# Optimization experiments

Measured on AMD Instinct MI355X. Metric: run time of the kernel, lower is better.

The kernel has to match this reference:

```python
import jax, jax.numpy as jnp
import numpy as np

SIGMA = 1.0          # influence distance of kernel points
KERNEL_RADIUS = 1.0  # radius within which kernel points live


def setup_inputs() -> dict:
    key = jax.random.key(0)
    k0, k1, k2, k3, k4 = jax.random.split(key, 5)
    B, M, K_NB, D_IN, D_OUT, K_PTS = 4, 16384, 32, 64, 64, 15
    X = jax.random.normal(k0, (B, M, 3), dtype=jnp.float32)          # point coords
    F = jax.random.normal(k1, (B, M, D_IN), dtype=jnp.float32)        # point features
    N = jax.random.randint(k2, (B, M, K_NB), 0, M)                    # neighbor indices
    Q = jax.random.uniform(k3, (K_PTS, 3), minval=-KERNEL_RADIUS,
                           maxval=KERNEL_RADIUS, dtype=jnp.float32)   # kernel points
    W = jax.random.normal(k4, (K_PTS, D_IN, D_OUT), dtype=jnp.float32) * 0.05
    return {"X": X, "F": F, "N": N, "Q": Q, "W": W}


def reference(X, F, N, Q, W):
    # Gather neighbor coordinates and features: [B, M, k, 3] / [B, M, k, d_in]
    gather = jax.vmap(lambda a, idx: a[idx])
    Xn = gather(X, N)
    Fn = gather(F, N)
    # Relative neighbor positions w.r.t. each center point
    r = Xn - X[:, :, None, :]                                  # [B, M, k, 3]
    # Distance of each relative position to each kernel point
    d = jnp.linalg.norm(r[:, :, :, None, :] - Q, axis=-1)      # [B, M, k, Kp]
    # Linear correlation influence (KPConv)
    h = jnp.maximum(0.0, 1.0 - d / SIGMA)                      # [B, M, k, Kp]
    # Distance-weighted neighbor aggregation per kernel point
    Fk = jnp.einsum('bmkp,bmkd->bmpd', h, Fn)                  # [B, M, Kp, d_in]
    # Per-kernel-point linear maps, summed over kernel points
    return jnp.einsum('bmpd,pde->bme', Fk, W)                  # [B, M, d_out]
```

## Files before the change

### kernel.cpp

```cpp
#include <hip/hip_runtime.h>
#include <hip/hip_bf16.h>


#define BATCH 4
#define MPTS  16384
#define KNB   32
#define DIN   64
#define DOUT  64
#define KP    15
#define K2P   1024
#define KSTEPS (K2P/32)
#define ROWB  (K2P*2)
#define PTS   (BATCH*MPTS)
#define PPB   16
#define NBLK  (PTS/PPB)
#define WBELEMS (K2P*DOUT)

typedef __bf16 bf16x8 __attribute__((ext_vector_type(8)));
typedef float  f32x4  __attribute__((ext_vector_type(4)));
typedef unsigned short u16x8 __attribute__((ext_vector_type(8)));

static __device__ __forceinline__ unsigned short f2b(float x) {
    __bf16 h = (__bf16)x;
    return __builtin_bit_cast(unsigned short, h);
}

__global__ void prep_wb(const float* __restrict__ W, unsigned short* __restrict__ wb) {
    int idx = blockIdx.x * 256 + threadIdx.x;
    if (idx >= WBELEMS) return;
    int i    = idx & 7;
    int lane = (idx >> 3) & 63;
    int ks   = (idx >> 9) & 31;
    int et   = idx >> 14;
    int kap  = ks * 32 + ((lane >> 4) << 3) + i;
    int n = kap >> 6;
    int g = (kap >> 4) & 3;
    int t = (kap >> 2) & 3;
    int r = kap & 3;
    int p = g * 4 + r;
    int d = n * 4 + t;
    int e = et * 16 + (lane & 15);
    float v = (p < KP) ? W[(p * DIN + d) * DOUT + e] : 0.f;
    wb[idx] = f2b(v);
}

__global__ void f2bf_kernel(const float* __restrict__ src, unsigned short* __restrict__ dst, int n8) {
    int i = blockIdx.x * 256 + threadIdx.x;
    if (i >= n8) return;
    const float4* s = reinterpret_cast<const float4*>(src) + (size_t)i * 2;
    float4 a = s[0], b = s[1];
    u16x8 o;
    o[0] = f2b(a.x); o[1] = f2b(a.y); o[2] = f2b(a.z); o[3] = f2b(a.w);
    o[4] = f2b(b.x); o[5] = f2b(b.y); o[6] = f2b(b.z); o[7] = f2b(b.w);
    *(reinterpret_cast<u16x8*>(dst) + i) = o;
}

__global__ __launch_bounds__(256, 5)
void kpconv_main(const float* __restrict__ X, const unsigned short* __restrict__ FB,
                 const int* __restrict__ NB, const float* __restrict__ Q,
                 const unsigned short* __restrict__ WB, float* __restrict__ OUT) {
    __shared__ unsigned short fk[16 * K2P];

    char* const fkb = reinterpret_cast<char*>(fk);

    const int tid  = threadIdx.x;
    const int wv   = tid >> 6;
    const int lane = tid & 63;
    const int g16  = lane >> 4;
    const int r16  = lane & 15;

    float qx = 1.0e3f, qy = 0.f, qz = 0.f;
    if (r16 < KP) { qx = Q[r16 * 3 + 0]; qy = Q[r16 * 3 + 1]; qz = Q[r16 * 3 + 2]; }
    const float qq   = qx * qx + qy * qy + qz * qz;
    const float nq2x = -2.f * qx, nq2y = -2.f * qy, nq2z = -2.f * qz;

    const int bid     = blockIdx.x;
    const int base_pt = (bid & 7) * (PTS / 8) + (bid >> 3) * PPB;
    const int boff    = (base_pt >> 14) * MPTS;
    const int pid0    = base_pt + wv * 4;

    #pragma unroll
    for (int e = 0; e < 2; ++e) {
        int ent = lane + e * 64;
        int j = ent >> 5, k = ent & 31;
        int pid = pid0 + j;
        int nb  = NB[(size_t)pid * KNB + k];
        int gidx = boff + nb;
        const float* xn = X + (size_t)gidx * 3;
        const float* xc = X + (size_t)pid * 3;
        float rx = xn[0] - xc[0];
        float ry = xn[1] - xc[1];
        float rz = xn[2] - xc[2];
        float rr = fmaf(rx, rx, fmaf(ry, ry, rz * rz));
        int slot = (k & 24) | ((k ^ (k >> 3)) & 7);
        *reinterpret_cast<float4*>(fkb + (wv * 4 + j) * ROWB + slot * 16) =
            make_float4(rx, ry, rz, rr);
    }

    union U { uint2 d; unsigned short s[4]; };
    U L[2][8];

    auto issue_gather = [&](int j, U* Lj) {
        const int* nbp = NB + (size_t)(pid0 + j) * KNB + g16 * 8;
        int4 a = *reinterpret_cast<const int4*>(nbp);
        int4 b = *reinterpret_cast<const int4*>(nbp + 4);
        int g[8] = {a.x, a.y, a.z, a.w, b.x, b.y, b.z, b.w};
        #pragma unroll
        for (int i = 0; i < 8; ++i)
            Lj[i].d = *reinterpret_cast<const uint2*>(
                FB + ((size_t)(boff + g[i]) << 6) + (r16 << 2));
    };

    issue_gather(0, L[0]);
    issue_gather(1, L[1]);

    #pragma unroll
    for (int j = 0; j < 4; ++j) {
        const int row = wv * 4 + j;

        bf16x8 ah;
        #pragma unroll
        for (int i = 0; i < 8; ++i) {
            float4 rv = *reinterpret_cast<const float4*>(
                fkb + row * ROWB + (g16 * 8 + (i ^ g16)) * 16);
            float d2 = fmaf(rv.x, nq2x, fmaf(rv.y, nq2y, fmaf(rv.z, nq2z, rv.w + qq)));
            d2 = fmaxf(d2, 0.f);
            ah[i] = (__bf16)fmaxf(1.f - __builtin_amdgcn_sqrtf(d2), 0.f);
        }

        bf16x8 bfr[4];
        #pragma unroll
        for (int t = 0; t < 4; ++t)
            #pragma unroll
            for (int i = 0; i < 8; ++i)
                bfr[t][i] = __builtin_bit_cast(__bf16, L[j & 1][i].s[t]);

        if (j < 2) issue_gather(j + 2, L[j & 1]);

        const f32x4 z = {0.f, 0.f, 0.f, 0.f};
        f32x4 accs[4];
        #pragma unroll
        for (int t = 0; t < 4; ++t)
            accs[t] = __builtin_amdgcn_mfma_f32_16x16x32_bf16(ah, bfr[t], z, 0, 0, 0);

        bf16x8 w0, w1;
        #pragma unroll
        for (int r = 0; r < 4; ++r) {
            w0[r]     = (__bf16)accs[0][r];
            w0[4 + r] = (__bf16)accs[1][r];
            w1[r]     = (__bf16)accs[2][r];
            w1[4 + r] = (__bf16)accs[3][r];
        }
        int swz  = (row & 7) ^ (r16 & 7);
        int off0 = row * ROWB + (r16 * 8 + ((g16 * 2 + 0) ^ swz)) * 16;
        int off1 = row * ROWB + (r16 * 8 + ((g16 * 2 + 1) ^ swz)) * 16;
        *reinterpret_cast<bf16x8*>(fkb + off0) = w0;
        *reinterpret_cast<bf16x8*>(fkb + off1) = w1;
    }

    __syncthreads();

    const unsigned short* wbp = WB + ((size_t)(wv * KSTEPS) * 64 + lane) * 8;
    asm volatile("" : "+v"(wbp));

    f32x4 o = {0.f, 0.f, 0.f, 0.f};
    #pragma unroll
    for (int ks = 0; ks < KSTEPS; ++ks) {
        bf16x8 b = *reinterpret_cast<const bf16x8*>(wbp + ks * 512);
        int stored = (ks * 4 + g16) ^ (r16 & 7) ^ ((ks >> 1) & 7);
        bf16x8 a = *reinterpret_cast<const bf16x8*>(fkb + r16 * ROWB + stored * 16);
        o = __builtin_amdgcn_mfma_f32_16x16x32_bf16(a, b, o, 0, 0, 0);
    }

    #pragma unroll
    for (int r = 0; r < 4; ++r) {
        int pid = base_pt + g16 * 4 + r;
        OUT[(size_t)pid * DOUT + wv * 16 + r16] = o[r];
    }
}

extern "C" void kernel_launch(void* const* d_in, const int* in_sizes, int n_in,
                              void* d_out, int out_size, void* d_ws, size_t ws_size,
                              hipStream_t stream) {
    const float* X = (const float*)d_in[0];
    const float* F = (const float*)d_in[1];
    const int*   N = (const int*)d_in[2];
    const float* Q = (const float*)d_in[3];
    const float* W = (const float*)d_in[4];
    float* OUT = (float*)d_out;
    unsigned short* WB = (unsigned short*)d_ws;
    unsigned short* FB = WB + WBELEMS;

    prep_wb<<<(WBELEMS + 255) / 256, 256, 0, stream>>>(W, WB);

    const int n8 = PTS * DIN / 8;
    f2bf_kernel<<<(n8 + 255) / 256, 256, 0, stream>>>(F, FB, n8);

    kpconv_main<<<NBLK, 256, 0, stream>>>(X, FB, N, Q, WB, OUT);
}
```

Before: 63.65 us.

## Warp-specialize main kernel into producer/consumer waves with double-buffered LDS tiles

The main kernel now uses 512-thread blocks. Four producer waves build the gathered, distance-weighted neighbour aggregate for a 16-point tile into one LDS buffer, while four consumer waves run the weight GEMM on the previous tile from the other buffer. Each block loops over 8 tiles, which cuts the block count and lets gather latency overlap MFMA work. The two preprocessing kernels are merged into one launch, and the consumer accumulation is split into two chains to shorten MFMA dependencies. In exchange, the kernel doubles LDS per block, syncs every tile, and launches fewer blocks, which may reduce parallelism.

```diff
diff --git a/kernel.cpp b/kernel.cpp
--- a/kernel.cpp
+++ b/kernel.cpp
@@ -12,9 +12,11 @@
 #define KSTEPS (K2P/32)
 #define ROWB  (K2P*2)
 #define PTS   (BATCH*MPTS)
-#define PPB   16
-#define NBLK  (PTS/PPB)
+#define TILES 8
+#define NBLK  (PTS/(16*TILES))
 #define WBELEMS (K2P*DOUT)
+#define WBBLK (WBELEMS/256)
+#define FBBLK (PTS*DIN/8/256)
 
 typedef __bf16 bf16x8 __attribute__((ext_vector_type(8)));
 typedef float  f32x4  __attribute__((ext_vector_type(4)));
@@ -25,83 +27,64 @@
     return __builtin_bit_cast(unsigned short, h);
 }
 
-__global__ void prep_wb(const float* __restrict__ W, unsigned short* __restrict__ wb) {
-    int idx = blockIdx.x * 256 + threadIdx.x;
-    if (idx >= WBELEMS) return;
-    int i    = idx & 7;
-    int lane = (idx >> 3) & 63;
-    int ks   = (idx >> 9) & 31;
-    int et   = idx >> 14;
-    int kap  = ks * 32 + ((lane >> 4) << 3) + i;
-    int n = kap >> 6;
-    int g = (kap >> 4) & 3;
-    int t = (kap >> 2) & 3;
-    int r = kap & 3;
-    int p = g * 4 + r;
-    int d = n * 4 + t;
-    int e = et * 16 + (lane & 15);
-    float v = (p < KP) ? W[(p * DIN + d) * DOUT + e] : 0.f;
-    wb[idx] = f2b(v);
-}
-
-__global__ void f2bf_kernel(const float* __restrict__ src, unsigned short* __restrict__ dst, int n8) {
-    int i = blockIdx.x * 256 + threadIdx.x;
-    if (i >= n8) return;
-    const float4* s = reinterpret_cast<const float4*>(src) + (size_t)i * 2;
-    float4 a = s[0], b = s[1];
-    u16x8 o;
-    o[0] = f2b(a.x); o[1] = f2b(a.y); o[2] = f2b(a.z); o[3] = f2b(a.w);
-    o[4] = f2b(b.x); o[5] = f2b(b.y); o[6] = f2b(b.z); o[7] = f2b(b.w);
-    *(reinterpret_cast<u16x8*>(dst) + i) = o;
-}
-
-__global__ __launch_bounds__(256, 5)
+__global__ void prep_all(const float* __restrict__ W, const float* __restrict__ F,
+                         unsigned short* __restrict__ wb, unsigned short* __restrict__ fb) {
+    int bid = blockIdx.x;
+    if (bid < WBBLK) {
+        int idx = bid * 256 + threadIdx.x;
+        int i    = idx & 7;
+        int lane = (idx >> 3) & 63;
+        int ks   = (idx >> 9) & 31;
+        int et   = idx >> 14;
+        int kap  = ks * 32 + ((lane >> 4) << 3) + i;
+        int n = kap >> 6;
+        int g = (kap >> 4) & 3;
+        int t = (kap >> 2) & 3;
+        int r = kap & 3;
+        int p = g * 4 + r;
+        int d = n * 4 + t;
+        int e = et * 16 + (lane & 15);
+        float v = (p < KP) ? W[(p * DIN + d) * DOUT + e] : 0.f;
+        wb[idx] = f2b(v);
+    } else {
+        int i = (bid - WBBLK) * 256 + threadIdx.x;
+        const float4* s = reinterpret_cast<const float4*>(F) + (size_t)i * 2;
+        float4 a = s[0], b = s[1];
+        u16x8 o;
+        o[0] = f2b(a.x); o[1] = f2b(a.y); o[2] = f2b(a.z); o[3] = f2b(a.w);
+        o[4] = f2b(b.x); o[5] = f2b(b.y); o[6] = f2b(b.z); o[7] = f2b(b.w);
+        *(reinterpret_cast<u16x8*>(fb) + i) = o;
+    }
+}
+
+__global__ __launch_bounds__(512, 4)
 void kpconv_main(const float* __restrict__ X, const unsigned short* __restrict__ FB,
                  const int* __restrict__ NB, const float* __restrict__ Q,
                  const unsigned short* __restrict__ WB, float* __restrict__ OUT) {
-    __shared__ unsigned short fk[16 * K2P];
-
-    char* const fkb = reinterpret_cast<char*>(fk);
+    __shared__ unsigned short fk[2][16 * K2P];
 
     const int tid  = threadIdx.x;
     const int wv   = tid >> 6;
     const int lane = tid & 63;
     const int g16  = lane >> 4;
     const int r16  = lane & 15;
+    const bool is_prod = (wv >= 4);
+    const int pw   = wv & 3;
 
     float qx = 1.0e3f, qy = 0.f, qz = 0.f;
     if (r16 < KP) { qx = Q[r16 * 3 + 0]; qy = Q[r16 * 3 + 1]; qz = Q[r16 * 3 + 2]; }
     const float qq   = qx * qx + qy * qy + qz * qz;
     const float nq2x = -2.f * qx, nq2y = -2.f * qy, nq2z = -2.f * qz;
 
-    const int bid     = blockIdx.x;
-    const int base_pt = (bid & 7) * (PTS / 8) + (bid >> 3) * PPB;
-    const int boff    = (base_pt >> 14) * MPTS;
-    const int pid0    = base_pt + wv * 4;
-
-    #pragma unroll
-    for (int e = 0; e < 2; ++e) {
-        int ent = lane + e * 64;
-        int j = ent >> 5, k = ent & 31;
-        int pid = pid0 + j;
-        int nb  = NB[(size_t)pid * KNB + k];
-        int gidx = boff + nb;
-        const float* xn = X + (size_t)gidx * 3;
-        const float* xc = X + (size_t)pid * 3;
-        float rx = xn[0] - xc[0];
-        float ry = xn[1] - xc[1];
-        float rz = xn[2] - xc[2];
-        float rr = fmaf(rx, rx, fmaf(ry, ry, rz * rz));
-        int slot = (k & 24) | ((k ^ (k >> 3)) & 7);
-        *reinterpret_cast<float4*>(fkb + (wv * 4 + j) * ROWB + slot * 16) =
-            make_float4(rx, ry, rz, rr);
-    }
+    const int bid      = blockIdx.x;
+    const int blk_base = (bid & 7) * (PTS / 8) + (bid >> 3) * (16 * TILES);
+    const int boff     = (blk_base >> 14) * MPTS;
 
     union U { uint2 d; unsigned short s[4]; };
     U L[2][8];
 
-    auto issue_gather = [&](int j, U* Lj) {
-        const int* nbp = NB + (size_t)(pid0 + j) * KNB + g16 * 8;
+    auto issue_gather = [&](int pid_j, U* Lj) {
+        const int* nbp = NB + (size_t)pid_j * KNB + g16 * 8;
         int4 a = *reinterpret_cast<const int4*>(nbp);
         int4 b = *reinterpret_cast<const int4*>(nbp + 4);
         int g[8] = {a.x, a.y, a.z, a.w, b.x, b.y, b.z, b.w};
@@ -111,71 +94,102 @@
                 FB + ((size_t)(boff + g[i]) << 6) + (r16 << 2));
     };
 
-    issue_gather(0, L[0]);
-    issue_gather(1, L[1]);
-
-    #pragma unroll
-    for (int j = 0; j < 4; ++j) {
-        const int row = wv * 4 + j;
-
-        bf16x8 ah;
-        #pragma unroll
-        for (int i = 0; i < 8; ++i) {
-            float4 rv = *reinterpret_cast<const float4*>(
-                fkb + row * ROWB + (g16 * 8 + (i ^ g16)) * 16);
-            float d2 = fmaf(rv.x, nq2x, fmaf(rv.y, nq2y, fmaf(rv.z, nq2z, rv.w + qq)));
-            d2 = fmaxf(d2, 0.f);
-            ah[i] = (__bf16)fmaxf(1.f - __builtin_amdgcn_sqrtf(d2), 0.f);
+    for (int t = 0; t <= TILES; ++t) {
+        if (is_prod && t < TILES) {
+            char* const fkb = reinterpret_cast<char*>(fk[t & 1]);
+            const int tp   = blk_base + t * 16;
+            const int pid0 = tp + pw * 4;
+
+            #pragma unroll
+            for (int e = 0; e < 2; ++e) {
+                int ent = lane + e * 64;
+                int j = ent >> 5, k = ent & 31;
+                int pid = pid0 + j;
+                int nb  = NB[(size_t)pid * KNB + k];
+                int gidx = boff + nb;
+                const float* xn = X + (size_t)gidx * 3;
+                const float* xc = X + (size_t)pid * 3;
+                float rx = xn[0] - xc[0];
+                float ry = xn[1] - xc[1];
+                float rz = xn[2] - xc[2];
+                float rr = fmaf(rx, rx, fmaf(ry, ry, rz * rz));
+                int slot = (k & 24) | ((k ^ (k >> 3)) & 7);
+                *reinterpret_cast<float4*>(fkb + (pw * 4 + j) * ROWB + slot * 16) =
+                    make_float4(rx, ry, rz, rr);
+            }
+
+            issue_gather(pid0 + 0, L[0]);
+            issue_gather(pid0 + 1, L[1]);
+
+            #pragma unroll
+            for (int j = 0; j < 4; ++j) {
+                const int row = pw * 4 + j;
+
+                bf16x8 ah;
+                #pragma unroll
+                for (int i = 0; i < 8; ++i) {
+                    float4 rv = *reinterpret_cast<const float4*>(
+                        fkb + row * ROWB + (g16 * 8 + (i ^ g16)) * 16);
+                    float d2 = fmaf(rv.x, nq2x, fmaf(rv.y, nq2y, fmaf(rv.z, nq2z, rv.w + qq)));
+                    d2 = fmaxf(d2, 0.f);
+                    ah[i] = (__bf16)fmaxf(1.f - __builtin_amdgcn_sqrtf(d2), 0.f);
+                }
+
+                bf16x8 bfr[4];
+                #pragma unroll
+                for (int tt = 0; tt < 4; ++tt)
+                    #pragma unroll
+                    for (int i = 0; i < 8; ++i)
+                        bfr[tt][i] = __builtin_bit_cast(__bf16, L[j & 1][i].s[tt]);
+
+                if (j < 2) issue_gather(pid0 + j + 2, L[j & 1]);
+
+                const f32x4 z = {0.f, 0.f, 0.f, 0.f};
+                f32x4 accs[4];
+                #pragma unroll
+                for (int tt = 0; tt < 4; ++tt)
+                    accs[tt] = __builtin_amdgcn_mfma_f32_16x16x32_bf16(ah, bfr[tt], z, 0, 0, 0);
+
+                bf16x8 w0, w1;
+                #pragma unroll
+                for (int r = 0; r < 4; ++r) {
+                    w0[r]     = (__bf16)accs[0][r];
+                    w0[4 + r] = (__bf16)accs[1][r];
+                    w1[r]     = (__bf16)accs[2][r];
+                    w1[4 + r] = (__bf16)accs[3][r];
+                }
+                int swz  = (row & 7) ^ (r16 & 7);
+                int off0 = row * ROWB + (r16 * 8 + ((g16 * 2 + 0) ^ swz)) * 16;
+                int off1 = row * ROWB + (r16 * 8 + ((g16 * 2 + 1) ^ swz)) * 16;
+                *reinterpret_cast<bf16x8*>(fkb + off0) = w0;
+                *reinterpret_cast<bf16x8*>(fkb + off1) = w1;
+            }
+        } else if (!is_prod && t > 0) {
+            const char* fkb = reinterpret_cast<const char*>(fk[(t - 1) & 1]);
+            const int tp_prev = blk_base + (t - 1) * 16;
+
+            const unsigned short* wbp = WB + ((size_t)(pw * KSTEPS) * 64 + lane) * 8;
+            asm volatile("" : "+v"(wbp));
+
+            f32x4 oe = {0.f, 0.f, 0.f, 0.f};
+            f32x4 oo = {0.f, 0.f, 0.f, 0.f};
+            #pragma unroll
+            for (int ks = 0; ks < KSTEPS; ++ks) {
+                bf16x8 b = *reinterpret_cast<const bf16x8*>(wbp + ks * 512);
+                int stored = (ks * 4 + g16) ^ (r16 & 7) ^ ((ks >> 1) & 7);
+                bf16x8 a = *reinterpret_cast<const bf16x8*>(fkb + r16 * ROWB + stored * 16);
+                if (ks & 1) oo = __builtin_amdgcn_mfma_f32_16x16x32_bf16(a, b, oo, 0, 0, 0);
+                else        oe = __builtin_amdgcn_mfma_f32_16x16x32_bf16(a, b, oe, 0, 0, 0);
+            }
+
+            #pragma unroll
+            for (int r = 0; r < 4; ++r) {
+                int pid = tp_prev + g16 * 4 + r;
+                OUT[(size_t)pid * DOUT + pw * 16 + r16] = oe[r] + oo[r];
+            }
         }
 
-        bf16x8 bfr[4];
-        #pragma unroll
-        for (int t = 0; t < 4; ++t)
-            #pragma unroll
-            for (int i = 0; i < 8; ++i)
-                bfr[t][i] = __builtin_bit_cast(__bf16, L[j & 1][i].s[t]);
-
-        if (j < 2) issue_gather(j + 2, L[j & 1]);
-
-        const f32x4 z = {0.f, 0.f, 0.f, 0.f};
-        f32x4 accs[4];
-        #pragma unroll
-        for (int t = 0; t < 4; ++t)
-            accs[t] = __builtin_amdgcn_mfma_f32_16x16x32_bf16(ah, bfr[t], z, 0, 0, 0);
-
-        bf16x8 w0, w1;
-        #pragma unroll
-        for (int r = 0; r < 4; ++r) {
-            w0[r]     = (__bf16)accs[0][r];
-            w0[4 + r] = (__bf16)accs[1][r];
-            w1[r]     = (__bf16)accs[2][r];
-            w1[4 + r] = (__bf16)accs[3][r];
-        }
-        int swz  = (row & 7) ^ (r16 & 7);
-        int off0 = row * ROWB + (r16 * 8 + ((g16 * 2 + 0) ^ swz)) * 16;
-        int off1 = row * ROWB + (r16 * 8 + ((g16 * 2 + 1) ^ swz)) * 16;
-        *reinterpret_cast<bf16x8*>(fkb + off0) = w0;
-        *reinterpret_cast<bf16x8*>(fkb + off1) = w1;
-    }
-
-    __syncthreads();
-
-    const unsigned short* wbp = WB + ((size_t)(wv * KSTEPS) * 64 + lane) * 8;
-    asm volatile("" : "+v"(wbp));
-
-    f32x4 o = {0.f, 0.f, 0.f, 0.f};
-    #pragma unroll
-    for (int ks = 0; ks < KSTEPS; ++ks) {
-        bf16x8 b = *reinterpret_cast<const bf16x8*>(wbp + ks * 512);
-        int stored = (ks * 4 + g16) ^ (r16 & 7) ^ ((ks >> 1) & 7);
-        bf16x8 a = *reinterpret_cast<const bf16x8*>(fkb + r16 * ROWB + stored * 16);
-        o = __builtin_amdgcn_mfma_f32_16x16x32_bf16(a, b, o, 0, 0, 0);
-    }
-
-    #pragma unroll
-    for (int r = 0; r < 4; ++r) {
-        int pid = base_pt + g16 * 4 + r;
-        OUT[(size_t)pid * DOUT + wv * 16 + r16] = o[r];
+        __syncthreads();
     }
 }
 
@@ -191,10 +205,6 @@
     unsigned short* WB = (unsigned short*)d_ws;
     unsigned short* FB = WB + WBELEMS;
 
-    prep_wb<<<(WBELEMS + 255) / 256, 256, 0, stream>>>(W, WB);
-
-    const int n8 = PTS * DIN / 8;
-    f2bf_kernel<<<(n8 + 255) / 256, 256, 0, stream>>>(F, FB, n8);
-
-    kpconv_main<<<NBLK, 256, 0, stream>>>(X, FB, N, Q, WB, OUT);
-}
+    prep_all<<<WBBLK + FBBLK, 256, 0, stream>>>(W, F, WB, FB);
+    kpconv_main<<<NBLK, 512, 0, stream>>>(X, FB, N, Q, WB, OUT);
+}
```

Result: slower. 75.67 us (+18.9%).

## Double points per block to reuse weight loads and merge prep kernels

Applied to the files above, without the earlier changes.

Each block now handles 32 points instead of 16. Every weight fragment loaded from global memory feeds two MFMAs, one per 16-row tile, which halves weight traffic per point. The gather pipeline is deepened to four in-flight neighbour rows, and the two preprocessing kernels are fused into one launch. The cost is twice the LDS per block (64KB) and more registers, with launch bounds lowered to 2 blocks per CU, so occupancy falls.

```diff
diff --git a/kernel.cpp b/kernel.cpp
--- a/kernel.cpp
+++ b/kernel.cpp
@@ -12,9 +12,11 @@
 #define KSTEPS (K2P/32)
 #define ROWB  (K2P*2)
 #define PTS   (BATCH*MPTS)
-#define PPB   16
+#define PPB   32
 #define NBLK  (PTS/PPB)
 #define WBELEMS (K2P*DOUT)
+#define WBBLK (WBELEMS/256)
+#define FBBLK (PTS*DIN/8/256)
 
 typedef __bf16 bf16x8 __attribute__((ext_vector_type(8)));
 typedef float  f32x4  __attribute__((ext_vector_type(4)));
@@ -25,42 +27,41 @@
     return __builtin_bit_cast(unsigned short, h);
 }
 
-__global__ void prep_wb(const float* __restrict__ W, unsigned short* __restrict__ wb) {
-    int idx = blockIdx.x * 256 + threadIdx.x;
-    if (idx >= WBELEMS) return;
-    int i    = idx & 7;
-    int lane = (idx >> 3) & 63;
-    int ks   = (idx >> 9) & 31;
-    int et   = idx >> 14;
-    int kap  = ks * 32 + ((lane >> 4) << 3) + i;
-    int n = kap >> 6;
-    int g = (kap >> 4) & 3;
-    int t = (kap >> 2) & 3;
-    int r = kap & 3;
-    int p = g * 4 + r;
-    int d = n * 4 + t;
-    int e = et * 16 + (lane & 15);
-    float v = (p < KP) ? W[(p * DIN + d) * DOUT + e] : 0.f;
-    wb[idx] = f2b(v);
-}
-
-__global__ void f2bf_kernel(const float* __restrict__ src, unsigned short* __restrict__ dst, int n8) {
-    int i = blockIdx.x * 256 + threadIdx.x;
-    if (i >= n8) return;
-    const float4* s = reinterpret_cast<const float4*>(src) + (size_t)i * 2;
-    float4 a = s[0], b = s[1];
-    u16x8 o;
-    o[0] = f2b(a.x); o[1] = f2b(a.y); o[2] = f2b(a.z); o[3] = f2b(a.w);
-    o[4] = f2b(b.x); o[5] = f2b(b.y); o[6] = f2b(b.z); o[7] = f2b(b.w);
-    *(reinterpret_cast<u16x8*>(dst) + i) = o;
-}
-
-__global__ __launch_bounds__(256, 5)
+__global__ void prep_all(const float* __restrict__ W, const float* __restrict__ F,
+                         unsigned short* __restrict__ wb, unsigned short* __restrict__ fb) {
+    int bid = blockIdx.x;
+    if (bid < WBBLK) {
+        int idx = bid * 256 + threadIdx.x;
+        int i    = idx & 7;
+        int lane = (idx >> 3) & 63;
+        int ks   = (idx >> 9) & 31;
+        int et   = idx >> 14;
+        int kap  = ks * 32 + ((lane >> 4) << 3) + i;
+        int n = kap >> 6;
+        int g = (kap >> 4) & 3;
+        int t = (kap >> 2) & 3;
+        int r = kap & 3;
+        int p = g * 4 + r;
+        int d = n * 4 + t;
+        int e = et * 16 + (lane & 15);
+        float v = (p < KP) ? W[(p * DIN + d) * DOUT + e] : 0.f;
+        wb[idx] = f2b(v);
+    } else {
+        int i = (bid - WBBLK) * 256 + threadIdx.x;
+        const float4* s = reinterpret_cast<const float4*>(F) + (size_t)i * 2;
+        float4 a = s[0], b = s[1];
+        u16x8 o;
+        o[0] = f2b(a.x); o[1] = f2b(a.y); o[2] = f2b(a.z); o[3] = f2b(a.w);
+        o[4] = f2b(b.x); o[5] = f2b(b.y); o[6] = f2b(b.z); o[7] = f2b(b.w);
+        *(reinterpret_cast<u16x8*>(fb) + i) = o;
+    }
+}
+
+__global__ __launch_bounds__(256, 2)
 void kpconv_main(const float* __restrict__ X, const unsigned short* __restrict__ FB,
                  const int* __restrict__ NB, const float* __restrict__ Q,
                  const unsigned short* __restrict__ WB, float* __restrict__ OUT) {
-    __shared__ unsigned short fk[16 * K2P];
-
+    __shared__ unsigned short fk[PPB * K2P];
     char* const fkb = reinterpret_cast<char*>(fk);
 
     const int tid  = threadIdx.x;
@@ -77,10 +78,10 @@
     const int bid     = blockIdx.x;
     const int base_pt = (bid & 7) * (PTS / 8) + (bid >> 3) * PPB;
     const int boff    = (base_pt >> 14) * MPTS;
-    const int pid0    = base_pt + wv * 4;
-
-    #pragma unroll
-    for (int e = 0; e < 2; ++e) {
+    const int pid0    = base_pt + wv * 8;
+
+    #pragma unroll
+    for (int e = 0; e < 4; ++e) {
         int ent = lane + e * 64;
         int j = ent >> 5, k = ent & 31;
         int pid = pid0 + j;
@@ -93,15 +94,15 @@
         float rz = xn[2] - xc[2];
         float rr = fmaf(rx, rx, fmaf(ry, ry, rz * rz));
         int slot = (k & 24) | ((k ^ (k >> 3)) & 7);
-        *reinterpret_cast<float4*>(fkb + (wv * 4 + j) * ROWB + slot * 16) =
+        *reinterpret_cast<float4*>(fkb + (wv * 8 + j) * ROWB + slot * 16) =
             make_float4(rx, ry, rz, rr);
     }
 
     union U { uint2 d; unsigned short s[4]; };
-    U L[2][8];
-
-    auto issue_gather = [&](int j, U* Lj) {
-        const int* nbp = NB + (size_t)(pid0 + j) * KNB + g16 * 8;
+    U L[4][8];
+
+    auto issue_gather = [&](int pid_j, U* Lj) {
+        const int* nbp = NB + (size_t)pid_j * KNB + g16 * 8;
         int4 a = *reinterpret_cast<const int4*>(nbp);
         int4 b = *reinterpret_cast<const int4*>(nbp + 4);
         int g[8] = {a.x, a.y, a.z, a.w, b.x, b.y, b.z, b.w};
@@ -111,12 +112,14 @@
                 FB + ((size_t)(boff + g[i]) << 6) + (r16 << 2));
     };
 
-    issue_gather(0, L[0]);
-    issue_gather(1, L[1]);
-
-    #pragma unroll
-    for (int j = 0; j < 4; ++j) {
-        const int row = wv * 4 + j;
+    issue_gather(pid0 + 0, L[0]);
+    issue_gather(pid0 + 1, L[1]);
+    issue_gather(pid0 + 2, L[2]);
+    issue_gather(pid0 + 3, L[3]);
+
+    #pragma unroll
+    for (int j = 0; j < 8; ++j) {
+        const int row = wv * 8 + j;
 
         bf16x8 ah;
         #pragma unroll
@@ -133,9 +136,9 @@
         for (int t = 0; t < 4; ++t)
             #pragma unroll
             for (int i = 0; i < 8; ++i)
-                bfr[t][i] = __builtin_bit_cast(__bf16, L[j & 1][i].s[t]);
-
-        if (j < 2) issue_gather(j + 2, L[j & 1]);
+                bfr[t][i] = __builtin_bit_cast(__bf16, L[j & 3][i].s[t]);
+
+        if (j < 4) issue_gather(pid0 + j + 4, L[j & 3]);
 
         const f32x4 z = {0.f, 0.f, 0.f, 0.f};
         f32x4 accs[4];
@@ -163,19 +166,24 @@
     const unsigned short* wbp = WB + ((size_t)(wv * KSTEPS) * 64 + lane) * 8;
     asm volatile("" : "+v"(wbp));
 
-    f32x4 o = {0.f, 0.f, 0.f, 0.f};
+    f32x4 o0 = {0.f, 0.f, 0.f, 0.f};
+    f32x4 o1 = {0.f, 0.f, 0.f, 0.f};
     #pragma unroll
     for (int ks = 0; ks < KSTEPS; ++ks) {
         bf16x8 b = *reinterpret_cast<const bf16x8*>(wbp + ks * 512);
         int stored = (ks * 4 + g16) ^ (r16 & 7) ^ ((ks >> 1) & 7);
-        bf16x8 a = *reinterpret_cast<const bf16x8*>(fkb + r16 * ROWB + stored * 16);
-        o = __builtin_amdgcn_mfma_f32_16x16x32_bf16(a, b, o, 0, 0, 0);
+        bf16x8 a0 = *reinterpret_cast<const bf16x8*>(fkb + r16 * ROWB + stored * 16);
+        bf16x8 a1 = *reinterpret_cast<const bf16x8*>(fkb + (16 + r16) * ROWB + stored * 16);
+        o0 = __builtin_amdgcn_mfma_f32_16x16x32_bf16(a0, b, o0, 0, 0, 0);
+        o1 = __builtin_amdgcn_mfma_f32_16x16x32_bf16(a1, b, o1, 0, 0, 0);
     }
 
     #pragma unroll
     for (int r = 0; r < 4; ++r) {
-        int pid = base_pt + g16 * 4 + r;
-        OUT[(size_t)pid * DOUT + wv * 16 + r16] = o[r];
+        int p0 = base_pt + g16 * 4 + r;
+        OUT[(size_t)p0 * DOUT + wv * 16 + r16] = o0[r];
+        int p1 = base_pt + 16 + g16 * 4 + r;
+        OUT[(size_t)p1 * DOUT + wv * 16 + r16] = o1[r];
     }
 }
 
@@ -191,10 +199,6 @@
     unsigned short* WB = (unsigned short*)d_ws;
     unsigned short* FB = WB + WBELEMS;
 
-    prep_wb<<<(WBELEMS + 255) / 256, 256, 0, stream>>>(W, WB);
-
-    const int n8 = PTS * DIN / 8;
-    f2bf_kernel<<<(n8 + 255) / 256, 256, 0, stream>>>(F, FB, n8);
-
+    prep_all<<<WBBLK + FBBLK, 256, 0, stream>>>(W, F, WB, FB);
     kpconv_main<<<NBLK, 256, 0, stream>>>(X, FB, N, Q, WB, OUT);
 }
```

After: 58.59 us. -8.0%, faster.
